# Kernel tuning notes

Hardware: AMD Instinct MI355X
Metric: run time of the kernel (lower is better)

The kernel has to match this reference:

```python
import jax, jax.numpy as jnp
import numpy as np


def setup_inputs() -> dict:
    key = jax.random.key(0)
    k1, k2 = jax.random.split(key)
    shape = (64, 1000000)
    x = jax.random.normal(k1, shape, dtype=jnp.float32)
    y = jax.random.normal(k2, shape, dtype=jnp.float32)
    return {"x": x, "y": y}


def reference(x, y):
    # loss = count(x_i < y_i) / n ; return 1 - loss
    xf = jnp.ravel(x)
    yf = jnp.ravel(y)
    win_rate = jnp.mean((xf < yf).astype(xf.dtype))
    return 1.0 - win_rate
```

## Files before the change

### kernel.cpp

```cpp
#include <hip/hip_runtime.h>

__global__ __launch_bounds__(256) void wrr_count_kernel(
    const float4* __restrict__ x, const float4* __restrict__ y,
    unsigned int* __restrict__ cnt, int n4) {
    int tid    = blockIdx.x * blockDim.x + threadIdx.x;
    int stride = gridDim.x * blockDim.x;

    unsigned int c = 0;
    for (int i = tid; i < n4; i += stride) {
        float4 a = x[i];
        float4 b = y[i];
        c += (a.x < b.x);
        c += (a.y < b.y);
        c += (a.z < b.z);
        c += (a.w < b.w);
    }

    #pragma unroll
    for (int off = 32; off > 0; off >>= 1)
        c += __shfl_down(c, off);

    __shared__ unsigned int s[4];
    int lane = threadIdx.x & 63;
    int wave = threadIdx.x >> 6;
    if (lane == 0) s[wave] = c;
    __syncthreads();
    if (threadIdx.x == 0) {
        unsigned int t = s[0] + s[1] + s[2] + s[3];
        atomicAdd(cnt, t);
    }
}

__global__ void wrr_finalize_kernel(const unsigned int* __restrict__ cnt,
                                    float* __restrict__ out, float inv_n) {
    out[0] = 1.0f - (float)(*cnt) * inv_n;
}

extern "C" void kernel_launch(void* const* d_in, const int* in_sizes, int n_in,
                              void* d_out, int out_size, void* d_ws, size_t ws_size,
                              hipStream_t stream) {
    const float* x = (const float*)d_in[0];
    const float* y = (const float*)d_in[1];
    float* out = (float*)d_out;
    unsigned int* cnt = (unsigned int*)d_ws;

    const long long n = (long long)in_sizes[0];
    const int n4 = (int)(n / 4);

    hipMemsetAsync(cnt, 0, sizeof(unsigned int), stream);

    const int block = 256;
    const int grid  = 2048;
    wrr_count_kernel<<<grid, block, 0, stream>>>(
        (const float4*)x, (const float4*)y, cnt, n4);

    wrr_finalize_kernel<<<1, 1, 0, stream>>>(cnt, out, 1.0f / (float)n);
}
```

Before: 100.8 us.

## Replace atomic accumulation and memset with per-block partials and parallel finalize

Each block now writes its count to a per-block slot in the workspace, and a 256-thread finalize kernel reduces those slots. This removes the memset launch and the global atomic. The main loop runs over a compile-time trip count with unroll 4 plus a single tail iteration, which gives more loads in flight. The cost is a slightly larger finalize kernel that reads 2048 partials.

Result: slower. 114.7 us (+13.8%).

```diff
diff --git a/kernel.cpp b/kernel.cpp
--- a/kernel.cpp
+++ b/kernel.cpp
@@ -1,39 +1,56 @@
 #include <hip/hip_runtime.h>
 
-__global__ __launch_bounds__(256) void wrr_count_kernel(
+#define WRR_GRID  2048
+#define WRR_BLOCK 256
+
+__global__ __launch_bounds__(WRR_BLOCK) void wrr_count_kernel(
     const float4* __restrict__ x, const float4* __restrict__ y,
-    unsigned int* __restrict__ cnt, int n4) {
-    int tid    = blockIdx.x * blockDim.x + threadIdx.x;
-    int stride = gridDim.x * blockDim.x;
+    unsigned int* __restrict__ partial, int n4) {
+    const int tid    = blockIdx.x * WRR_BLOCK + threadIdx.x;
+    const int stride = WRR_GRID * WRR_BLOCK;
 
     unsigned int c = 0;
-    for (int i = tid; i < n4; i += stride) {
+    const int full = n4 / stride;
+    int i = tid;
+    #pragma unroll 4
+    for (int j = 0; j < full; ++j, i += stride) {
         float4 a = x[i];
         float4 b = y[i];
-        c += (a.x < b.x);
-        c += (a.y < b.y);
-        c += (a.z < b.z);
-        c += (a.w < b.w);
+        c += (unsigned)(a.x < b.x) + (unsigned)(a.y < b.y) +
+             (unsigned)(a.z < b.z) + (unsigned)(a.w < b.w);
+    }
+    if (i < n4) {
+        float4 a = x[i];
+        float4 b = y[i];
+        c += (unsigned)(a.x < b.x) + (unsigned)(a.y < b.y) +
+             (unsigned)(a.z < b.z) + (unsigned)(a.w < b.w);
     }
 
     #pragma unroll
     for (int off = 32; off > 0; off >>= 1)
         c += __shfl_down(c, off);
 
-    __shared__ unsigned int s[4];
-    int lane = threadIdx.x & 63;
-    int wave = threadIdx.x >> 6;
-    if (lane == 0) s[wave] = c;
+    __shared__ unsigned int s[WRR_BLOCK / 64];
+    if ((threadIdx.x & 63) == 0) s[threadIdx.x >> 6] = c;
     __syncthreads();
-    if (threadIdx.x == 0) {
-        unsigned int t = s[0] + s[1] + s[2] + s[3];
-        atomicAdd(cnt, t);
-    }
+    if (threadIdx.x == 0)
+        partial[blockIdx.x] = s[0] + s[1] + s[2] + s[3];
 }
 
-__global__ void wrr_finalize_kernel(const unsigned int* __restrict__ cnt,
-                                    float* __restrict__ out, float inv_n) {
-    out[0] = 1.0f - (float)(*cnt) * inv_n;
+__global__ __launch_bounds__(256) void wrr_finalize_kernel(
+    const unsigned int* __restrict__ partial, float* __restrict__ out,
+    float inv_n) {
+    unsigned int c = 0;
+    for (int i = threadIdx.x; i < WRR_GRID; i += 256)
+        c += partial[i];
+    #pragma unroll
+    for (int off = 32; off > 0; off >>= 1)
+        c += __shfl_down(c, off);
+    __shared__ unsigned int s[4];
+    if ((threadIdx.x & 63) == 0) s[threadIdx.x >> 6] = c;
+    __syncthreads();
+    if (threadIdx.x == 0)
+        out[0] = 1.0f - (float)(s[0] + s[1] + s[2] + s[3]) * inv_n;
 }
 
 extern "C" void kernel_launch(void* const* d_in, const int* in_sizes, int n_in,
@@ -42,17 +59,12 @@
     const float* x = (const float*)d_in[0];
     const float* y = (const float*)d_in[1];
     float* out = (float*)d_out;
-    unsigned int* cnt = (unsigned int*)d_ws;
+    unsigned int* partial = (unsigned int*)d_ws;
 
     const long long n = (long long)in_sizes[0];
     const int n4 = (int)(n / 4);
 
-    hipMemsetAsync(cnt, 0, sizeof(unsigned int), stream);
-
-    const int block = 256;
-    const int grid  = 2048;
-    wrr_count_kernel<<<grid, block, 0, stream>>>(
-        (const float4*)x, (const float4*)y, cnt, n4);
-
-    wrr_finalize_kernel<<<1, 1, 0, stream>>>(cnt, out, 1.0f / (float)n);
+    wrr_count_kernel<<<WRR_GRID, WRR_BLOCK, 0, stream>>>(
+        (const float4*)x, (const float4*)y, partial, n4);
+    wrr_finalize_kernel<<<1, 256, 0, stream>>>(partial, out, 1.0f / (float)n);
 }
```
